# Performance work log

Measured on AMD Instinct MI355X. Metric: run time of the kernel, lower is better.

The kernel has to match this reference:

```python
import jax, jax.numpy as jnp
import numpy as np

B, IN_DIM, Q_DIM, CODE_DIM, K, PROJ_DIM = 8192, 512, 128, 1024, 8, 64
NUM_LAYERS = 5
THRESHOLD = 0.9
SPARSITY_LEVELS = list(map(int, np.linspace(5, CODE_DIM, K)))  # matches torch default


def setup_inputs() -> dict:
    key = jax.random.key(0)
    ks = jax.random.split(key, 9)
    s = 0.02
    return {
        "x": jax.random.normal(ks[0], (B, IN_DIM), jnp.float32),
        "Wq": jax.random.normal(ks[1], (IN_DIM, Q_DIM), jnp.float32) * s,
        "bq": jnp.zeros((Q_DIM,), jnp.float32),
        "keys": jax.random.normal(ks[2], (K, Q_DIM), jnp.float32) * s,
        "We": jax.random.normal(ks[3], (K, IN_DIM, CODE_DIM), jnp.float32) * s,
        "S": jax.random.normal(ks[4], (K, CODE_DIM, CODE_DIM), jnp.float32) * s,
        "theta": jax.random.uniform(ks[5], (K,), jnp.float32) * 0.01,
        "W1": jax.random.normal(ks[6], (CODE_DIM, CODE_DIM), jnp.float32) * s,
        "b1": jnp.zeros((CODE_DIM,), jnp.float32),
        "W2": jax.random.normal(ks[7], (CODE_DIM, PROJ_DIM), jnp.float32) * s,
        "b2": jnp.zeros((PROJ_DIM,), jnp.float32),
    }


def _soft(z, theta):
    return jnp.sign(z) * jnp.maximum(jnp.abs(z) - theta, 0.0)


def reference(x, Wq, bq, keys, We, S, theta, W1, b1, W2, b2):
    # --- gating (attention): softmax(q @ keys^T / sqrt(d)) -> (B, K)
    q = x @ Wq + bq
    scores = (q @ keys.T) / jnp.sqrt(jnp.asarray(Q_DIM, x.dtype))
    gating_probs = jax.nn.softmax(scores, axis=-1)

    # --- all K LISTA experts densely: zs has shape (K, B, code_dim)
    Bx = jnp.einsum('bi,kic->kbc', x, We)            # (K, B, C)
    th = theta[:, None, None]
    z = _soft(Bx, th)
    for _ in range(NUM_LAYERS):
        z = _soft(Bx + jnp.einsum('kbc,kcd->kbd', z, S), th)

    # hard top-k (sparsity_level) magnitude pruning per expert
    pruned = []
    for k in range(K):
        zk = z[k]
        kk = SPARSITY_LEVELS[k]
        az = jnp.abs(zk)
        kth = jax.lax.top_k(az, kk)[0][:, -1]         # (B,)
        pruned.append(jnp.where(az >= kth[:, None], zk, 0.0))
    zs = jnp.stack(pruned, axis=0)                    # (K, B, C)

    # --- hard gating: among experts with p >= threshold*p_max, pick the
    # one with the smallest sparsity level (argmax always eligible, so the
    # empty-eligible branch in the torch code is unreachable for threshold<=1)
    p_max = jnp.max(gating_probs, axis=-1, keepdims=True)
    eligible = gating_probs >= THRESHOLD * p_max      # (B, K)
    sl = jnp.asarray(SPARSITY_LEVELS, jnp.float32)
    idx = jnp.argmin(jnp.where(eligible, sl[None, :], jnp.inf), axis=-1)  # (B,)

    selected_z = jnp.take_along_axis(zs, idx[None, :, None], axis=0)[0]   # (B, C)

    # --- projection head
    h = jax.nn.relu(selected_z @ W1 + b1)
    return h @ W2 + b2
```

## Files before the change

kernel.cpp:

```cpp
#include <hip/hip_runtime.h>
#include <math.h>

#define NB 8192
#define IND 512
#define QDIM 128
#define CD 1024
#define KE 8
#define PD 64
#define PCAP 160

typedef _Float16 h8 __attribute__((ext_vector_type(8)));
typedef _Float16 h4 __attribute__((ext_vector_type(4)));
typedef float fx16 __attribute__((ext_vector_type(16)));

#define GLD16(g, l) __builtin_amdgcn_global_load_lds((const __attribute__((address_space(1))) void*)(g), (__attribute__((address_space(3))) void*)(l), 16, 0, 0)

__device__ __forceinline__ float softt(float v, float th) {
    float a = fabsf(v) - th;
    return a > 0.0f ? copysignf(a, v) : 0.0f;
}

__device__ __forceinline__ void fsplit(float v, _Float16& hi, _Float16& lo) {
    hi = (_Float16)v;
    lo = (_Float16)((v - (float)hi) * 2048.0f);
}

__global__ void k_precompute_M(const float* __restrict__ Wq, const float* __restrict__ keys,
                               const float* __restrict__ bq, float* __restrict__ M,
                               float* __restrict__ sb) {
    const float RSQ = 0.088388347648318447f;
    int g = blockIdx.x * 256 + threadIdx.x;
    if (g < IND * KE) {
        int i = g >> 3, k = g & 7;
        float s = 0.f;
        for (int q = 0; q < QDIM; ++q) s += Wq[i * QDIM + q] * keys[k * QDIM + q];
        M[g] = s * RSQ;
    }
    if (blockIdx.x == 0 && threadIdx.x < KE) {
        int k = threadIdx.x;
        float s = 0.f;
        for (int q = 0; q < QDIM; ++q) s += bq[q] * keys[k * QDIM + q];
        sb[k] = s * RSQ;
    }
}

__global__ __launch_bounds__(256)
void k_scores(const float* __restrict__ x, const float* __restrict__ M,
              const float* __restrict__ sb, int* __restrict__ idx) {
    __shared__ float Ms[KE][IND];
    __shared__ float sbs[KE];
    int t = threadIdx.x;
    #pragma unroll
    for (int j = 0; j < 16; ++j) {
        int e = j * 256 + t;
        Ms[e & 7][e >> 3] = M[e];
    }
    if (t < KE) sbs[t] = sb[t];
    __syncthreads();
    int w = t >> 6, lane = t & 63;
    int row = blockIdx.x * 4 + w;
    const float* xr = x + (size_t)row * IND;
    float sc[KE];
    #pragma unroll
    for (int k = 0; k < KE; ++k) sc[k] = 0.f;
    #pragma unroll
    for (int j = 0; j < IND / 64; ++j) {
        int ii = lane + 64 * j;
        float xv = xr[ii];
        #pragma unroll
        for (int k = 0; k < KE; ++k) sc[k] += xv * Ms[k][ii];
    }
    #pragma unroll
    for (int k = 0; k < KE; ++k) {
        #pragma unroll
        for (int off = 32; off >= 1; off >>= 1) sc[k] += __shfl_down(sc[k], off, 64);
    }
    if (lane == 0) {
        float smax = -1e30f;
        #pragma unroll
        for (int k = 0; k < KE; ++k) { sc[k] += sbs[k]; smax = fmaxf(smax, sc[k]); }
        const float LN09 = -0.105360515657826301f;
        int e = 0;
        #pragma unroll
        for (int k = KE - 1; k >= 0; --k)
            if (sc[k] >= smax + LN09) e = k;
        idx[row] = e;
    }
}

__global__ __launch_bounds__(256)
void k_count(const int* __restrict__ idx, int* __restrict__ perm,
             int* __restrict__ counts, int* __restrict__ offsets) {
    __shared__ int hist[256][KE];
    __shared__ int sc[2][KE][256];
    __shared__ int base[KE];
    const int t = threadIdx.x;
    int pc[KE];
    #pragma unroll
    for (int e = 0; e < KE; ++e) pc[e] = 0;
    for (int j = 0; j < NB / 256; ++j) pc[idx[j * 256 + t]]++;
    #pragma unroll
    for (int e = 0; e < KE; ++e) { hist[t][e] = pc[e]; sc[0][e][t] = pc[e]; }
    __syncthreads();
    int cur = 0;
    for (int d = 1; d < 256; d <<= 1) {
        #pragma unroll
        for (int e = 0; e < KE; ++e) {
            int v = sc[cur][e][t];
            if (t >= d) v += sc[cur][e][t - d];
            sc[cur ^ 1][e][t] = v;
        }
        cur ^= 1;
        __syncthreads();
    }
    if (t == 0) {
        int a = 0;
        #pragma unroll
        for (int e = 0; e < KE; ++e) {
            int tot = sc[cur][e][255];
            base[e] = a; offsets[e] = a; counts[e] = tot; a += tot;
        }
    }
    __syncthreads();
    int pos[KE];
    #pragma unroll
    for (int e = 0; e < KE; ++e) pos[e] = base[e] + sc[cur][e][t] - hist[t][e];
    for (int j = 0; j < NB / 256; ++j) {
        int r = j * 256 + t;
        int e = idx[r];
        perm[pos[e]++] = r;
    }
}

__global__ __launch_bounds__(256)
void k_split_rows(const float* __restrict__ src, _Float16* __restrict__ ph,
                  _Float16* __restrict__ pl, int n) {
    int i = (blockIdx.x * 256 + threadIdx.x) * 4;
    if (i < n) {
        float4 v = *(const float4*)(src + i);
        h4 hh, ll;
        #pragma unroll
        for (int j = 0; j < 4; ++j) {
            _Float16 a, b;
            fsplit((&v.x)[j], a, b);
            hh[j] = a; ll[j] = b;
        }
        *(h4*)(ph + i) = hh;
        *(h4*)(pl + i) = ll;
    }
}

__global__ __launch_bounds__(256)
void k_tsplit(const float* __restrict__ src, _Float16* __restrict__ th,
              _Float16* __restrict__ tl, int K, const int* __restrict__ counts) {
    int e = blockIdx.z;
    if (counts[e] == 0) return;
    __shared__ float tile[64][65];
    int k0 = blockIdx.x * 64;
    int n0 = blockIdx.y * 64;
    const float* s = src + (size_t)e * K * CD;
    int t = threadIdx.x;
    int tr = t >> 4;
    int tc = (t & 15) * 4;
    #pragma unroll
    for (int p = 0; p < 4; ++p) {
        int kk = tr + p * 16;
        float4 v = *(const float4*)&s[(size_t)(k0 + kk) * CD + n0 + tc];
        #pragma unroll
        for (int j = 0; j < 4; ++j) tile[kk][tc + j] = (&v.x)[j];
    }
    __syncthreads();
    int n = t >> 2;
    int kq = (t & 3) * 16;
    h8 hh0, hh1, ll0, ll1;
    #pragma unroll
    for (int j = 0; j < 8; ++j) {
        _Float16 a, b;
        fsplit(tile[kq + j][n], a, b);
        hh0[j] = a; ll0[j] = b;
        fsplit(tile[kq + 8 + j][n], a, b);
        hh1[j] = a; ll1[j] = b;
    }
    size_t ob = ((size_t)e * CD + n0 + n) * K + k0 + kq;
    *(h8*)(th + ob) = hh0;
    *(h8*)(th + ob + 8) = hh1;
    *(h8*)(tl + ob) = ll0;
    *(h8*)(tl + ob + 8) = ll1;
}

template <int KDIM, int MODE>
__global__ __launch_bounds__(512, 4)
void k_mfma(const _Float16* __restrict__ Ah, const _Float16* __restrict__ Al,
            const _Float16* __restrict__ Bh, const _Float16* __restrict__ Bl,
            const float* __restrict__ theta, const float* __restrict__ BxBuf,
            float* __restrict__ BxOut, _Float16* __restrict__ zh, _Float16* __restrict__ zl,
            float* __restrict__ zf,
            const int* __restrict__ perm, const int* __restrict__ counts,
            const int* __restrict__ offsets) {
    const int e = blockIdx.z;
    const int cnt = counts[e];
    const int p = blockIdx.x + 8 * blockIdx.y;
    const int gx = p & 7;
    const int qq = p >> 3;
    const int bxl = qq & 7;
    const int byl = gx + 8 * (qq >> 3);
    const int m0 = byl * 128;
    if (m0 >= cnt) return;
    const int n0 = bxl * 128;
    const int off = offsets[e];
    const float th = theta[e];

    __shared__ _Float16 Asl[2][128 * 64];
    __shared__ _Float16 Bsl[2][128 * 64];

    const int t = threadIdx.x;
    const int lane = t & 63;
    const int w = t >> 6;

    const _Float16* aptr[2];
    const _Float16* bptr[2];
    #pragma unroll
    for (int i = 0; i < 2; ++i) {
        int s = w * 2 + i;
        int r = s * 8 + (lane >> 3);
        int pc = lane & 7;
        int lc = pc ^ ((r ^ (r >> 3)) & 7);
        int comp = lc & 1;
        int kg = lc >> 1;
        int mrow = m0 + r; if (mrow > cnt - 1) mrow = cnt - 1;
        size_t grow;
        if constexpr (MODE == 0) grow = (size_t)perm[off + mrow];
        else grow = (size_t)(off + mrow);
        aptr[i] = (comp ? Al : Ah) + grow * KDIM + kg * 8;
        bptr[i] = (comp ? Bl : Bh) + ((size_t)e * CD + n0 + r) * KDIM + kg * 8;
    }

    const int wm = w >> 1, wn = w & 1;
    const int q = lane >> 5;
    const int ml = lane & 31;

    fx16 acc[2];
    #pragma unroll
    for (int nt = 0; nt < 2; ++nt)
        #pragma unroll
        for (int g = 0; g < 16; ++g) acc[nt][g] = 0.f;

    auto stage = [&](int kt, int buf) {
        const int koff = kt * 32;
        #pragma unroll
        for (int i = 0; i < 2; ++i) {
            GLD16(aptr[i] + koff, &Asl[buf][(w * 2 + i) * 512]);
            GLD16(bptr[i] + koff, &Bsl[buf][(w * 2 + i) * 512]);
        }
    };

    const _Float16 SC = (_Float16)4.8828125e-4f;

    const int NT = KDIM / 32;
    stage(0, 0);
    stage(1, 1);
    asm volatile("s_waitcnt vmcnt(4)" ::: "memory");
    __builtin_amdgcn_sched_barrier(0);
    __builtin_amdgcn_s_barrier();

    for (int kt = 0; kt < NT; ++kt) {
        const int buf = kt & 1;
        h8 ah[2], al2[2], bh2[2][2], bl2[2][2];
        #pragma unroll
        for (int ks = 0; ks < 2; ++ks) {
            const int base = ks * 4 + q * 2;
            {
                int row = wm * 32 + ml;
                int sw = (row ^ (row >> 3)) & 7;
                int mb = row * 64;
                ah[ks]  = *(const h8*)&Asl[buf][mb + (((base + 0) ^ sw) * 8)];
                al2[ks] = *(const h8*)&Asl[buf][mb + (((base + 1) ^ sw) * 8)];
            }
            #pragma unroll
            for (int nt = 0; nt < 2; ++nt) {
                int col = wn * 64 + nt * 32 + ml;
                int sw = (col ^ (col >> 3)) & 7;
                int nb = col * 64;
                bh2[ks][nt] = *(const h8*)&Bsl[buf][nb + (((base + 0) ^ sw) * 8)];
                bl2[ks][nt] = *(const h8*)&Bsl[buf][nb + (((base + 1) ^ sw) * 8)];
            }
        }
        asm volatile("s_waitcnt lgkmcnt(0)" ::: "memory");
        __builtin_amdgcn_sched_barrier(0);
        __builtin_amdgcn_s_barrier();
        if (kt + 2 < NT) stage(kt + 2, buf);
        #pragma unroll
        for (int ks = 0; ks < 2; ++ks) {
            h8 ahs = ah[ks] * SC;
            h8 bhs[2];
            #pragma unroll
            for (int nt = 0; nt < 2; ++nt) bhs[nt] = bh2[ks][nt] * SC;
            #pragma unroll
            for (int nt = 0; nt < 2; ++nt) {
                acc[nt] = __builtin_amdgcn_mfma_f32_32x32x16_f16(ah[ks],  bh2[ks][nt], acc[nt], 0, 0, 0);
                acc[nt] = __builtin_amdgcn_mfma_f32_32x32x16_f16(ahs,     bl2[ks][nt], acc[nt], 0, 0, 0);
                acc[nt] = __builtin_amdgcn_mfma_f32_32x32x16_f16(al2[ks], bhs[nt],     acc[nt], 0, 0, 0);
            }
        }
        if (kt + 1 < NT) {
            if (kt + 2 < NT) {
                asm volatile("s_waitcnt vmcnt(4)" ::: "memory");
            } else {
                asm volatile("s_waitcnt vmcnt(0)" ::: "memory");
            }
            __builtin_amdgcn_sched_barrier(0);
            __builtin_amdgcn_s_barrier();
        }
    }

    #pragma unroll
    for (int nt = 0; nt < 2; ++nt) {
        #pragma unroll
        for (int g = 0; g < 16; ++g) {
            int rl = wm * 32 + (g & 3) + 8 * (g >> 2) + 4 * q;
            int mrow = m0 + rl;
            if (mrow < cnt) {
                int col = n0 + wn * 64 + nt * 32 + ml;
                size_t addr = (size_t)(off + mrow) * CD + col;
                float v = acc[nt][g];
                if constexpr (MODE == 0) {
                    BxOut[addr] = v;
                    float z = softt(v, th);
                    _Float16 a, b;
                    fsplit(z, a, b);
                    zh[addr] = a; zl[addr] = b;
                } else if constexpr (MODE == 1) {
                    float z = softt(v + BxBuf[addr], th);
                    _Float16 a, b;
                    fsplit(z, a, b);
                    zh[addr] = a; zl[addr] = b;
                } else {
                    zf[addr] = softt(v + BxBuf[addr], th);
                }
            }
        }
    }
}

__global__ __launch_bounds__(256)
void k_po(const float* __restrict__ z, const int* __restrict__ offsets,
          const float* __restrict__ W1, const float* __restrict__ b1,
          const float* __restrict__ W2, const float* __restrict__ b2,
          const int* __restrict__ perm, float* __restrict__ out) {
    const int SL[KE] = {5, 150, 296, 441, 587, 732, 878, 1024};
    __shared__ float vLg[4][PCAP];
    __shared__ int   iLg[4][PCAP];
    __shared__ float hSg[4][CD];
    __shared__ float prt[4][4][64];
    const int t = threadIdx.x;
    const int lane = t & 63;
    const int wv = t >> 6;
    const int slot = blockIdx.x * 4 + wv;
    float* vL = vLg[wv];
    int* iLs = iLg[wv];
    float* hS = hSg[wv];

    int k = 0;
    #pragma unroll
    for (int e = 1; e < KE; ++e)
        if (slot >= offsets[e]) k = e;
    const int lvl = SL[k];

    const float* zr = z + (size_t)slot * CD;
    float v[16];
    unsigned ab[16];
    #pragma unroll
    for (int j = 0; j < 16; ++j) {
        v[j] = zr[lane + 64 * j];
        ab[j] = __float_as_uint(fabsf(v[j]));
    }
    unsigned thr = 0;
    for (int b = 30; b >= 0; --b) {
        unsigned cand = thr | (1u << b);
        int c = 0;
        #pragma unroll
        for (int j = 0; j < 16; ++j)
            c += __popcll(__ballot(ab[j] >= cand));
        if (c >= lvl) {
            thr = cand;
            if (c == lvl) break;
        }
    }
    int cnt = 0;
    #pragma unroll
    for (int j = 0; j < 16; ++j) cnt += __popcll(__ballot(ab[j] >= thr));

    float h[16];
    #pragma unroll
    for (int j = 0; j < 16; ++j) h[j] = b1[lane + 64 * j];

    if (cnt <= PCAP) {
        int base = 0;
        #pragma unroll
        for (int j = 0; j < 16; ++j) {
            bool keep = ab[j] >= thr;
            unsigned long long m = __ballot(keep);
            if (keep) {
                int pos = base + __popcll(m & ((1ULL << lane) - 1));
                vL[pos] = v[j];
                iLs[pos] = lane + 64 * j;
            }
            base += __popcll(m);
        }
        __builtin_amdgcn_wave_barrier();
        for (int e = 0; e < cnt; ++e) {
            float val = vL[e];
            const float* wr = W1 + (size_t)iLs[e] * CD;
            #pragma unroll
            for (int j = 0; j < 16; ++j)
                h[j] = fmaf(val, wr[lane + 64 * j], h[j]);
        }
    } else {
        #pragma unroll
        for (int j = 0; j < 16; ++j)
            hS[lane + 64 * j] = (ab[j] >= thr) ? v[j] : 0.f;
        __builtin_amdgcn_wave_barrier();
        for (int e = 0; e < CD; ++e) {
            float val = hS[e];
            const float* wr = W1 + (size_t)e * CD;
            #pragma unroll
            for (int j = 0; j < 16; ++j)
                h[j] = fmaf(val, wr[lane + 64 * j], h[j]);
        }
        __builtin_amdgcn_wave_barrier();
    }

    #pragma unroll
    for (int j = 0; j < 16; ++j) hSg[wv][lane + 64 * j] = fmaxf(h[j], 0.f);
    __syncthreads();

    const float* w2c = W2 + lane;
    float a[4] = {0.f, 0.f, 0.f, 0.f};
    const int i0 = wv * 256;
    #pragma unroll 4
    for (int i = i0; i < i0 + 256; i += 4) {
        float w0 = w2c[(size_t)(i + 0) * PD];
        float w1 = w2c[(size_t)(i + 1) * PD];
        float w2v = w2c[(size_t)(i + 2) * PD];
        float w3 = w2c[(size_t)(i + 3) * PD];
        #pragma unroll
        for (int r = 0; r < 4; ++r) {
            float4 hv = *(const float4*)&hSg[r][i];
            a[r] = fmaf(hv.x, w0, a[r]);
            a[r] = fmaf(hv.y, w1, a[r]);
            a[r] = fmaf(hv.z, w2v, a[r]);
            a[r] = fmaf(hv.w, w3, a[r]);
        }
    }
    #pragma unroll
    for (int r = 0; r < 4; ++r) prt[wv][r][lane] = a[r];
    __syncthreads();

    float acc = ((prt[0][wv][lane] + prt[1][wv][lane]) +
                 (prt[2][wv][lane] + prt[3][wv][lane])) + b2[lane];
    out[(size_t)perm[slot] * PD + lane] = acc;
}

extern "C" void kernel_launch(void* const* d_in, const int* in_sizes, int n_in,
                              void* d_out, int out_size, void* d_ws, size_t ws_size,
                              hipStream_t stream) {
    const float* x     = (const float*)d_in[0];
    const float* Wq    = (const float*)d_in[1];
    const float* bq    = (const float*)d_in[2];
    const float* keys  = (const float*)d_in[3];
    const float* We    = (const float*)d_in[4];
    const float* S     = (const float*)d_in[5];
    const float* theta = (const float*)d_in[6];
    const float* W1    = (const float*)d_in[7];
    const float* b1    = (const float*)d_in[8];
    const float* W2    = (const float*)d_in[9];
    const float* b2    = (const float*)d_in[10];
    float* out = (float*)d_out;

    const size_t F = (size_t)NB * CD;
    float* Bx = (float*)d_ws;
    _Float16* zAh = (_Float16*)(Bx + F);
    _Float16* zAl = zAh + F;
    float* R1 = (float*)(zAl + F);
    _Float16* xh  = (_Float16*)R1;
    _Float16* xl  = xh + (size_t)NB * IND;
    _Float16* weh = xl + (size_t)NB * IND;
    _Float16* wel = weh + (size_t)KE * IND * CD;
    _Float16* zBh = (_Float16*)R1;
    _Float16* zBl = zBh + F;
    float* z1 = R1;
    _Float16* sth = (_Float16*)(R1 + F);
    _Float16* stl = sth + F;
    float* M  = (float*)(stl + F);
    float* sb = M + IND * KE;
    int* idx     = (int*)(sb + 8);
    int* perm    = idx + NB;
    int* counts  = perm + NB;
    int* offsets = counts + KE;

    k_precompute_M<<<16, 256, 0, stream>>>(Wq, keys, bq, M, sb);
    k_scores<<<NB / 4, 256, 0, stream>>>(x, M, sb, idx);
    k_count<<<1, 256, 0, stream>>>(idx, perm, counts, offsets);

    k_split_rows<<<(NB * IND) / 1024, 256, 0, stream>>>(x, xh, xl, NB * IND);
    {
        dim3 g(IND / 64, CD / 64, KE);
        k_tsplit<<<g, 256, 0, stream>>>(We, weh, wel, IND, counts);
    }
    {
        dim3 g(CD / 64, CD / 64, KE);
        k_tsplit<<<g, 256, 0, stream>>>(S, sth, stl, CD, counts);
    }

    dim3 gg(CD / 128, NB / 128, KE);
    k_mfma<IND, 0><<<gg, 512, 0, stream>>>(xh, xl, weh, wel, theta, nullptr, Bx, zAh, zAl, nullptr, perm, counts, offsets);
    k_mfma<CD, 1><<<gg, 512, 0, stream>>>(zAh, zAl, sth, stl, theta, Bx, nullptr, zBh, zBl, nullptr, perm, counts, offsets);
    k_mfma<CD, 1><<<gg, 512, 0, stream>>>(zBh, zBl, sth, stl, theta, Bx, nullptr, zAh, zAl, nullptr, perm, counts, offsets);
    k_mfma<CD, 1><<<gg, 512, 0, stream>>>(zAh, zAl, sth, stl, theta, Bx, nullptr, zBh, zBl, nullptr, perm, counts, offsets);
    k_mfma<CD, 1><<<gg, 512, 0, stream>>>(zBh, zBl, sth, stl, theta, Bx, nullptr, zAh, zAl, nullptr, perm, counts, offsets);
    k_mfma<CD, 2><<<gg, 512, 0, stream>>>(zAh, zAl, sth, stl, theta, Bx, nullptr, nullptr, nullptr, z1, perm, counts, offsets);

    k_po<<<NB / 4, 256, 0, stream>>>(z1, offsets, W1, b1, W2, b2, perm, out);
}
```

Before: 582.7 us.

## Split hi/lo accumulators and overlap LDS reads with first-half MFMAs

```diff
diff --git a/kernel.cpp b/kernel.cpp
--- a/kernel.cpp
+++ b/kernel.cpp
@@ -239,11 +239,11 @@
     const int q = lane >> 5;
     const int ml = lane & 31;
 
-    fx16 acc[2];
+    fx16 acc1[2], acc2[2];
     #pragma unroll
     for (int nt = 0; nt < 2; ++nt)
         #pragma unroll
-        for (int g = 0; g < 16; ++g) acc[nt][g] = 0.f;
+        for (int g = 0; g < 16; ++g) { acc1[nt][g] = 0.f; acc2[nt][g] = 0.f; }
 
     auto stage = [&](int kt, int buf) {
         const int koff = kt * 32;
@@ -253,8 +253,6 @@
             GLD16(bptr[i] + koff, &Bsl[buf][(w * 2 + i) * 512]);
         }
     };
-
-    const _Float16 SC = (_Float16)4.8828125e-4f;
 
     const int NT = KDIM / 32;
     stage(0, 0);
@@ -263,45 +261,64 @@
     __builtin_amdgcn_sched_barrier(0);
     __builtin_amdgcn_s_barrier();
 
+    const int arow = wm * 32 + ml;
+    const int asw = (arow ^ (arow >> 3)) & 7;
+    const int amb = arow * 64;
+
     for (int kt = 0; kt < NT; ++kt) {
         const int buf = kt & 1;
-        h8 ah[2], al2[2], bh2[2][2], bl2[2][2];
-        #pragma unroll
-        for (int ks = 0; ks < 2; ++ks) {
-            const int base = ks * 4 + q * 2;
-            {
-                int row = wm * 32 + ml;
-                int sw = (row ^ (row >> 3)) & 7;
-                int mb = row * 64;
-                ah[ks]  = *(const h8*)&Asl[buf][mb + (((base + 0) ^ sw) * 8)];
-                al2[ks] = *(const h8*)&Asl[buf][mb + (((base + 1) ^ sw) * 8)];
-            }
+        h8 ah0, al0, b0h[2], b0l[2];
+        {
+            const int base = 0 * 4 + q * 2;
+            ah0 = *(const h8*)&Asl[buf][amb + (((base + 0) ^ asw) * 8)];
+            al0 = *(const h8*)&Asl[buf][amb + (((base + 1) ^ asw) * 8)];
             #pragma unroll
             for (int nt = 0; nt < 2; ++nt) {
                 int col = wn * 64 + nt * 32 + ml;
                 int sw = (col ^ (col >> 3)) & 7;
                 int nb = col * 64;
-                bh2[ks][nt] = *(const h8*)&Bsl[buf][nb + (((base + 0) ^ sw) * 8)];
-                bl2[ks][nt] = *(const h8*)&Bsl[buf][nb + (((base + 1) ^ sw) * 8)];
+                b0h[nt] = *(const h8*)&Bsl[buf][nb + (((base + 0) ^ sw) * 8)];
+                b0l[nt] = *(const h8*)&Bsl[buf][nb + (((base + 1) ^ sw) * 8)];
             }
         }
+        __builtin_amdgcn_sched_barrier(0);
+        h8 ah1, al1, b1h[2], b1l[2];
+        {
+            const int base = 1 * 4 + q * 2;
+            ah1 = *(const h8*)&Asl[buf][amb + (((base + 0) ^ asw) * 8)];
+            al1 = *(const h8*)&Asl[buf][amb + (((base + 1) ^ asw) * 8)];
+            #pragma unroll
+            for (int nt = 0; nt < 2; ++nt) {
+                int col = wn * 64 + nt * 32 + ml;
+                int sw = (col ^ (col >> 3)) & 7;
+                int nb = col * 64;
+                b1h[nt] = *(const h8*)&Bsl[buf][nb + (((base + 0) ^ sw) * 8)];
+                b1l[nt] = *(const h8*)&Bsl[buf][nb + (((base + 1) ^ sw) * 8)];
+            }
+        }
+        __builtin_amdgcn_sched_barrier(0);
+        asm volatile("s_waitcnt lgkmcnt(6)" ::: "memory");
+        __builtin_amdgcn_sched_barrier(0);
+        __builtin_amdgcn_s_setprio(1);
+        #pragma unroll
+        for (int nt = 0; nt < 2; ++nt) {
+            acc1[nt] = __builtin_amdgcn_mfma_f32_32x32x16_f16(ah0, b0h[nt], acc1[nt], 0, 0, 0);
+            acc2[nt] = __builtin_amdgcn_mfma_f32_32x32x16_f16(ah0, b0l[nt], acc2[nt], 0, 0, 0);
+            acc2[nt] = __builtin_amdgcn_mfma_f32_32x32x16_f16(al0, b0h[nt], acc2[nt], 0, 0, 0);
+        }
+        __builtin_amdgcn_s_setprio(0);
         asm volatile("s_waitcnt lgkmcnt(0)" ::: "memory");
         __builtin_amdgcn_sched_barrier(0);
         __builtin_amdgcn_s_barrier();
         if (kt + 2 < NT) stage(kt + 2, buf);
-        #pragma unroll
-        for (int ks = 0; ks < 2; ++ks) {
-            h8 ahs = ah[ks] * SC;
-            h8 bhs[2];
-            #pragma unroll
-            for (int nt = 0; nt < 2; ++nt) bhs[nt] = bh2[ks][nt] * SC;
-            #pragma unroll
-            for (int nt = 0; nt < 2; ++nt) {
-                acc[nt] = __builtin_amdgcn_mfma_f32_32x32x16_f16(ah[ks],  bh2[ks][nt], acc[nt], 0, 0, 0);
-                acc[nt] = __builtin_amdgcn_mfma_f32_32x32x16_f16(ahs,     bl2[ks][nt], acc[nt], 0, 0, 0);
-                acc[nt] = __builtin_amdgcn_mfma_f32_32x32x16_f16(al2[ks], bhs[nt],     acc[nt], 0, 0, 0);
-            }
-        }
+        __builtin_amdgcn_s_setprio(1);
+        #pragma unroll
+        for (int nt = 0; nt < 2; ++nt) {
+            acc1[nt] = __builtin_amdgcn_mfma_f32_32x32x16_f16(ah1, b1h[nt], acc1[nt], 0, 0, 0);
+            acc2[nt] = __builtin_amdgcn_mfma_f32_32x32x16_f16(ah1, b1l[nt], acc2[nt], 0, 0, 0);
+            acc2[nt] = __builtin_amdgcn_mfma_f32_32x32x16_f16(al1, b1h[nt], acc2[nt], 0, 0, 0);
+        }
+        __builtin_amdgcn_s_setprio(0);
         if (kt + 1 < NT) {
             if (kt + 2 < NT) {
                 asm volatile("s_waitcnt vmcnt(4)" ::: "memory");
@@ -313,6 +330,7 @@
         }
     }
 
+    const float LSC = 4.8828125e-4f;
     #pragma unroll
     for (int nt = 0; nt < 2; ++nt) {
         #pragma unroll
@@ -322,7 +340,7 @@
             if (mrow < cnt) {
                 int col = n0 + wn * 64 + nt * 32 + ml;
                 size_t addr = (size_t)(off + mrow) * CD + col;
-                float v = acc[nt][g];
+                float v = acc1[nt][g] + acc2[nt][g] * LSC;
                 if constexpr (MODE == 0) {
                     BxOut[addr] = v;
                     float z = softt(v, th);
```

Result: slower. 722.5 us (+24.0%).

## Halve GEMM N-tile and split K across warp halves with LDS reduction

Applied to the files above, without the earlier changes.

```diff
diff --git a/kernel.cpp b/kernel.cpp
--- a/kernel.cpp
+++ b/kernel.cpp
@@ -189,7 +189,7 @@
 }
 
 template <int KDIM, int MODE>
-__global__ __launch_bounds__(512, 4)
+__global__ __launch_bounds__(512, 6)
 void k_mfma(const _Float16* __restrict__ Ah, const _Float16* __restrict__ Al,
             const _Float16* __restrict__ Bh, const _Float16* __restrict__ Bl,
             const float* __restrict__ theta, const float* __restrict__ BxBuf,
@@ -199,31 +199,32 @@
             const int* __restrict__ offsets) {
     const int e = blockIdx.z;
     const int cnt = counts[e];
-    const int p = blockIdx.x + 8 * blockIdx.y;
+    const int p = blockIdx.x + 16 * blockIdx.y;
     const int gx = p & 7;
     const int qq = p >> 3;
-    const int bxl = qq & 7;
-    const int byl = gx + 8 * (qq >> 3);
+    const int bxl = qq & 15;
+    const int byl = gx + 8 * (qq >> 4);
     const int m0 = byl * 128;
     if (m0 >= cnt) return;
-    const int n0 = bxl * 128;
+    const int n0 = bxl * 64;
     const int off = offsets[e];
     const float th = theta[e];
 
     __shared__ _Float16 Asl[2][128 * 64];
-    __shared__ _Float16 Bsl[2][128 * 64];
+    __shared__ _Float16 Bsl[2][64 * 64];
 
     const int t = threadIdx.x;
     const int lane = t & 63;
     const int w = t >> 6;
+    const int ks = w >> 2;
+    const int wm = w & 3;
 
     const _Float16* aptr[2];
-    const _Float16* bptr[2];
     #pragma unroll
     for (int i = 0; i < 2; ++i) {
-        int s = w * 2 + i;
-        int r = s * 8 + (lane >> 3);
-        int pc = lane & 7;
+        int idx = i * 512 + t;
+        int r = idx >> 3;
+        int pc = idx & 7;
         int lc = pc ^ ((r ^ (r >> 3)) & 7);
         int comp = lc & 1;
         int kg = lc >> 1;
@@ -232,10 +233,17 @@
         if constexpr (MODE == 0) grow = (size_t)perm[off + mrow];
         else grow = (size_t)(off + mrow);
         aptr[i] = (comp ? Al : Ah) + grow * KDIM + kg * 8;
-        bptr[i] = (comp ? Bl : Bh) + ((size_t)e * CD + n0 + r) * KDIM + kg * 8;
-    }
-
-    const int wm = w >> 1, wn = w & 1;
+    }
+    const _Float16* bptr;
+    {
+        int r = t >> 3;
+        int pc = t & 7;
+        int lc = pc ^ ((r ^ (r >> 3)) & 7);
+        int comp = lc & 1;
+        int kg = lc >> 1;
+        bptr = (comp ? Bl : Bh) + ((size_t)e * CD + n0 + r) * KDIM + kg * 8;
+    }
+
     const int q = lane >> 5;
     const int ml = lane & 31;
 
@@ -247,11 +255,9 @@
 
     auto stage = [&](int kt, int buf) {
         const int koff = kt * 32;
-        #pragma unroll
-        for (int i = 0; i < 2; ++i) {
-            GLD16(aptr[i] + koff, &Asl[buf][(w * 2 + i) * 512]);
-            GLD16(bptr[i] + koff, &Bsl[buf][(w * 2 + i) * 512]);
-        }
+        GLD16(aptr[0] + koff, &Asl[buf][w * 512]);
+        GLD16(aptr[1] + koff, &Asl[buf][4096 + w * 512]);
+        GLD16(bptr + koff, &Bsl[buf][w * 512]);
     };
 
     const _Float16 SC = (_Float16)4.8828125e-4f;
@@ -259,52 +265,47 @@
     const int NT = KDIM / 32;
     stage(0, 0);
     stage(1, 1);
-    asm volatile("s_waitcnt vmcnt(4)" ::: "memory");
+    asm volatile("s_waitcnt vmcnt(3)" ::: "memory");
     __builtin_amdgcn_sched_barrier(0);
     __builtin_amdgcn_s_barrier();
 
+    const int arow = wm * 32 + ml;
+    const int asw = (arow ^ (arow >> 3)) & 7;
+    const int amb = arow * 64;
+    const int base = ks * 4 + q * 2;
+
     for (int kt = 0; kt < NT; ++kt) {
         const int buf = kt & 1;
-        h8 ah[2], al2[2], bh2[2][2], bl2[2][2];
-        #pragma unroll
-        for (int ks = 0; ks < 2; ++ks) {
-            const int base = ks * 4 + q * 2;
-            {
-                int row = wm * 32 + ml;
-                int sw = (row ^ (row >> 3)) & 7;
-                int mb = row * 64;
-                ah[ks]  = *(const h8*)&Asl[buf][mb + (((base + 0) ^ sw) * 8)];
-                al2[ks] = *(const h8*)&Asl[buf][mb + (((base + 1) ^ sw) * 8)];
-            }
-            #pragma unroll
-            for (int nt = 0; nt < 2; ++nt) {
-                int col = wn * 64 + nt * 32 + ml;
-                int sw = (col ^ (col >> 3)) & 7;
-                int nb = col * 64;
-                bh2[ks][nt] = *(const h8*)&Bsl[buf][nb + (((base + 0) ^ sw) * 8)];
-                bl2[ks][nt] = *(const h8*)&Bsl[buf][nb + (((base + 1) ^ sw) * 8)];
-            }
+        h8 ah, al, bh2[2], bl2[2];
+        ah = *(const h8*)&Asl[buf][amb + (((base + 0) ^ asw) * 8)];
+        al = *(const h8*)&Asl[buf][amb + (((base + 1) ^ asw) * 8)];
+        #pragma unroll
+        for (int nt = 0; nt < 2; ++nt) {
+            int col = nt * 32 + ml;
+            int sw = (col ^ (col >> 3)) & 7;
+            int nb = col * 64;
+            bh2[nt] = *(const h8*)&Bsl[buf][nb + (((base + 0) ^ sw) * 8)];
+            bl2[nt] = *(const h8*)&Bsl[buf][nb + (((base + 1) ^ sw) * 8)];
         }
         asm volatile("s_waitcnt lgkmcnt(0)" ::: "memory");
         __builtin_amdgcn_sched_barrier(0);
         __builtin_amdgcn_s_barrier();
         if (kt + 2 < NT) stage(kt + 2, buf);
-        #pragma unroll
-        for (int ks = 0; ks < 2; ++ks) {
-            h8 ahs = ah[ks] * SC;
+        {
+            h8 ahs = ah * SC;
             h8 bhs[2];
             #pragma unroll
-            for (int nt = 0; nt < 2; ++nt) bhs[nt] = bh2[ks][nt] * SC;
+            for (int nt = 0; nt < 2; ++nt) bhs[nt] = bh2[nt] * SC;
             #pragma unroll
             for (int nt = 0; nt < 2; ++nt) {
-                acc[nt] = __builtin_amdgcn_mfma_f32_32x32x16_f16(ah[ks],  bh2[ks][nt], acc[nt], 0, 0, 0);
-                acc[nt] = __builtin_amdgcn_mfma_f32_32x32x16_f16(ahs,     bl2[ks][nt], acc[nt], 0, 0, 0);
-                acc[nt] = __builtin_amdgcn_mfma_f32_32x32x16_f16(al2[ks], bhs[nt],     acc[nt], 0, 0, 0);
+                acc[nt] = __builtin_amdgcn_mfma_f32_32x32x16_f16(ah,  bh2[nt], acc[nt], 0, 0, 0);
+                acc[nt] = __builtin_amdgcn_mfma_f32_32x32x16_f16(ahs, bl2[nt], acc[nt], 0, 0, 0);
+                acc[nt] = __builtin_amdgcn_mfma_f32_32x32x16_f16(al,  bhs[nt], acc[nt], 0, 0, 0);
             }
         }
         if (kt + 1 < NT) {
             if (kt + 2 < NT) {
-                asm volatile("s_waitcnt vmcnt(4)" ::: "memory");
+                asm volatile("s_waitcnt vmcnt(3)" ::: "memory");
             } else {
                 asm volatile("s_waitcnt vmcnt(0)" ::: "memory");
             }
@@ -313,29 +314,43 @@
         }
     }
 
-    #pragma unroll
-    for (int nt = 0; nt < 2; ++nt) {
-        #pragma unroll
-        for (int g = 0; g < 16; ++g) {
-            int rl = wm * 32 + (g & 3) + 8 * (g >> 2) + 4 * q;
-            int mrow = m0 + rl;
-            if (mrow < cnt) {
-                int col = n0 + wn * 64 + nt * 32 + ml;
-                size_t addr = (size_t)(off + mrow) * CD + col;
-                float v = acc[nt][g];
-                if constexpr (MODE == 0) {
-                    BxOut[addr] = v;
-                    float z = softt(v, th);
-                    _Float16 a, b;
-                    fsplit(z, a, b);
-                    zh[addr] = a; zl[addr] = b;
-                } else if constexpr (MODE == 1) {
-                    float z = softt(v + BxBuf[addr], th);
-                    _Float16 a, b;
-                    fsplit(z, a, b);
-                    zh[addr] = a; zl[addr] = b;
-                } else {
-                    zf[addr] = softt(v + BxBuf[addr], th);
+    float* pf = (float*)Asl;
+    if (ks == 1) {
+        #pragma unroll
+        for (int nt = 0; nt < 2; ++nt)
+            #pragma unroll
+            for (int g = 0; g < 16; ++g) {
+                int lr = (g & 3) + 8 * (g >> 2) + 4 * q;
+                pf[wm * 2048 + lr * 64 + nt * 32 + ml] = acc[nt][g];
+            }
+    }
+    __syncthreads();
+
+    if (ks == 0) {
+        #pragma unroll
+        for (int nt = 0; nt < 2; ++nt) {
+            #pragma unroll
+            for (int g = 0; g < 16; ++g) {
+                int lr = (g & 3) + 8 * (g >> 2) + 4 * q;
+                int mrow = m0 + wm * 32 + lr;
+                if (mrow < cnt) {
+                    int col = n0 + nt * 32 + ml;
+                    size_t addr = (size_t)(off + mrow) * CD + col;
+                    float v = acc[nt][g] + pf[wm * 2048 + lr * 64 + nt * 32 + ml];
+                    if constexpr (MODE == 0) {
+                        BxOut[addr] = v;
+                        float z = softt(v, th);
+                        _Float16 a, b;
+                        fsplit(z, a, b);
+                        zh[addr] = a; zl[addr] = b;
+                    } else if constexpr (MODE == 1) {
+                        float z = softt(v + BxBuf[addr], th);
+                        _Float16 a, b;
+                        fsplit(z, a, b);
+                        zh[addr] = a; zl[addr] = b;
+                    } else {
+                        zf[addr] = softt(v + BxBuf[addr], th);
+                    }
                 }
             }
         }
@@ -512,7 +527,7 @@
         k_tsplit<<<g, 256, 0, stream>>>(S, sth, stl, CD, counts);
     }
 
-    dim3 gg(CD / 128, NB / 128, KE);
+    dim3 gg(CD / 64, NB / 128, KE);
     k_mfma<IND, 0><<<gg, 512, 0, stream>>>(xh, xl, weh, wel, theta, nullptr, Bx, zAh, zAl, nullptr, perm, counts, offsets);
     k_mfma<CD, 1><<<gg, 512, 0, stream>>>(zAh, zAl, sth, stl, theta, Bx, nullptr, zBh, zBl, nullptr, perm, counts, offsets);
     k_mfma<CD, 1><<<gg, 512, 0, stream>>>(zBh, zBl, sth, stl, theta, Bx, nullptr, zAh, zAl, nullptr, perm, counts, offsets);
```

New measurement: 680.3 us. 16.8% more time.
